# Optimization experiments

Measured on AMD Instinct MI355X. Metric: run time of the kernel, lower is better.

## Reference

```python
import jax, jax.numpy as jnp
import numpy as np

T, B, F, H, O = 2048, 256, 64, 256, 1

def setup_inputs() -> dict:
    key = jax.random.key(0)
    k0, k1, k2 = jax.random.split(key, 3)
    return {
        "x": jax.random.normal(k0, (T, B, F), jnp.float32),          # (Time, Batch, Feat)
        "W0": jax.random.normal(k1, (H, F + H), jnp.float32) * 0.05,  # i2h weight (PyTorch layout)
        "b0": jnp.zeros((H,), jnp.float32),
        "Wfc": jax.random.normal(k2, (O, H), jnp.float32) * 0.05,     # fc1 weight
        "bfc": jnp.zeros((O,), jnp.float32),
        "feature_n": 0,
    }

def reference(x, W0, b0, Wfc, bfc, feature_n):
    # RnnCell: h = tanh(Linear(cat([x_t, h], 1))); then out_t = fc1(h).
    batch = x.shape[1]
    hidden = W0.shape[0]
    h0 = jnp.zeros((batch, hidden), x.dtype)

    def step(h, x_t):
        combined = jnp.concatenate([x_t, h], axis=1)          # (B, F+H)
        h_new = jnp.tanh(combined @ W0.T + b0)                # (B, H)
        out = h_new @ Wfc.T + bfc                             # (B, O)
        return h_new, out

    _, outs = jax.lax.scan(step, h0, x)                       # (T, B, O)
    # torch.stack(outputs, 1).squeeze(2) -> (B, T)
    return jnp.transpose(outs, (1, 0, 2)).squeeze(2)
```

## Files before the change

### kernel.cpp

```cpp
#include <hip/hip_runtime.h>

#define T_STEPS 2048
#define BATCH   256
#define FEAT    64
#define HID     256
#define KAUG    320
#define NW      16
#define NTHR    1024
#define XTILE   16
#define NXB     4
#define NTILES  (T_STEPS / XTILE)

typedef _Float16 half8 __attribute__((ext_vector_type(8)));
typedef float    f32x4 __attribute__((ext_vector_type(4)));
typedef float    f32x8 __attribute__((ext_vector_type(8)));

__device__ __forceinline__ float fast_tanh(float z) {
    float e = __expf(2.0f * z);
    return 1.0f - 2.0f * __builtin_amdgcn_rcpf(e + 1.0f);
}

__global__
__attribute__((amdgpu_flat_work_group_size(NTHR, NTHR), amdgpu_waves_per_eu(4, 4)))
void rnn_kernel(const float* __restrict__ x,
                const float* __restrict__ W0,
                const float* __restrict__ b0,
                const float* __restrict__ Wfc,
                const float* __restrict__ bfc,
                float* __restrict__ out)
{
    const int b    = blockIdx.x;
    const int tid  = threadIdx.x;
    const int w    = tid >> 6;
    const int lane = tid & 63;
    const int l15  = lane & 15;
    const int kg   = lane >> 4;
    const bool alane = (l15 == 0);

    __shared__ __align__(16) _Float16 h_buf[2][HID];
    __shared__ __align__(16) _Float16 x_tile[NXB][XTILE][FEAT];
    __shared__ __align__(16) float    out_buf[T_STEPS];

    half8 bw[10];
    {
        const float* wp = W0 + (16 * w + l15) * KAUG + kg * 8;
#pragma unroll
        for (int c = 0; c < 10; ++c) {
            const f32x8 v = *reinterpret_cast<const f32x8*>(wp + c * 32);
            bw[c] = __builtin_convertvector(v, half8);
        }
    }

    float b0e = 0.f, wfe = 0.f;
    if (lane < 16) {
        b0e = b0[16 * w + lane];
        wfe = Wfc[16 * w + lane];
    }
    const float bfc_r = bfc[0];

    if (tid < HID) { h_buf[0][tid] = (_Float16)0.f; h_buf[1][tid] = (_Float16)0.f; }
    out_buf[tid]        = bfc_r;
    out_buf[tid + NTHR] = bfc_r;

    const int tr = tid >> 6;
    const int fx = tid & 63;
#pragma unroll
    for (int ti = 0; ti < 2; ++ti) {
        const float v = x[(size_t)(XTILE * ti + tr) * (BATCH * FEAT) + b * FEAT + fx];
        x_tile[ti][tr][fx] = (_Float16)v;
    }
    float xhold = x[(size_t)(XTILE * 2 + tr) * (BATCH * FEAT) + b * FEAT + fx];
    __syncthreads();

    half8 af[10];
#pragma unroll
    for (int c = 0; c < 10; ++c) af[c] = half8{};

    float p_prev = 0.f;
    const f32x4 zero4 = {0.f, 0.f, 0.f, 0.f};

    for (int t = 0; t < T_STEPS; ++t) {
        const int cur = t & 1;
        const int nxt = cur ^ 1;
        const int xb  = (t >> 4) & (NXB - 1);

        if (alane) {
            const _Float16* xr = &x_tile[xb][t & 15][kg * 8];
            af[0] = *reinterpret_cast<const half8*>(xr);
            af[1] = *reinterpret_cast<const half8*>(xr + 32);
            const _Float16* hr = &h_buf[cur][kg * 8];
#pragma unroll
            for (int c = 2; c < 10; ++c)
                af[c] = *reinterpret_cast<const half8*>(hr + (c - 2) * 32);
        }

        {
            float p = p_prev;
            p += __shfl_xor(p, 1, 64);
            p += __shfl_xor(p, 2, 64);
            p += __shfl_xor(p, 4, 64);
            p += __shfl_xor(p, 8, 64);
            if (lane == 0 && t > 0) atomicAdd(&out_buf[t - 1], p);
        }

        f32x4 a0 = __builtin_amdgcn_mfma_f32_16x16x32_f16(af[0], bw[0], zero4, 0, 0, 0);
        f32x4 a1 = __builtin_amdgcn_mfma_f32_16x16x32_f16(af[1], bw[1], zero4, 0, 0, 0);
#pragma unroll
        for (int c = 2; c < 10; c += 2) {
            a0 = __builtin_amdgcn_mfma_f32_16x16x32_f16(af[c],     bw[c],     a0, 0, 0, 0);
            a1 = __builtin_amdgcn_mfma_f32_16x16x32_f16(af[c + 1], bw[c + 1], a1, 0, 0, 0);
        }

        if ((t & 15) == 0) {
            const int ti = t >> 4;
            if (ti + 2 < NTILES)
                x_tile[(ti + 2) & (NXB - 1)][tr][fx] = (_Float16)xhold;
            if (ti + 3 < NTILES)
                xhold = x[(size_t)(XTILE * (ti + 3) + tr) * (BATCH * FEAT) + b * FEAT + fx];
        }

        float pnew = 0.f;
        if (lane < 16) {
            const float h = fast_tanh(a0[0] + a1[0] + b0e);
            h_buf[nxt][16 * w + lane] = (_Float16)h;
            pnew = wfe * h;
        }
        p_prev = pnew;

        __syncthreads();
    }

    {
        float p = p_prev;
        p += __shfl_xor(p, 1, 64);
        p += __shfl_xor(p, 2, 64);
        p += __shfl_xor(p, 4, 64);
        p += __shfl_xor(p, 8, 64);
        if (lane == 0) atomicAdd(&out_buf[T_STEPS - 1], p);
    }
    __syncthreads();

    out[b * T_STEPS + tid]        = out_buf[tid];
    out[b * T_STEPS + tid + NTHR] = out_buf[tid + NTHR];
}

extern "C" void kernel_launch(void* const* d_in, const int* in_sizes, int n_in,
                              void* d_out, int out_size, void* d_ws, size_t ws_size,
                              hipStream_t stream) {
    const float* x   = (const float*)d_in[0];
    const float* W0  = (const float*)d_in[1];
    const float* b0  = (const float*)d_in[2];
    const float* Wfc = (const float*)d_in[3];
    const float* bfc = (const float*)d_in[4];
    float* out = (float*)d_out;

    rnn_kernel<<<dim3(BATCH), dim3(NTHR), 0, stream>>>(x, W0, b0, Wfc, bfc, out);
}
```

Baseline: 1.834 ms.

## Pack eight batch rows per block into MFMA rows with fewer, larger blocks

Each block now processes 8 batch elements at once, using 8 of the 16 MFMA A-matrix rows instead of one. Each of the 8 waves computes two 16-wide hidden tiles, so there are 32 blocks of 512 threads instead of 256 blocks of 1024. The fc output is now computed from the shared hidden state with a full-wave dot product and shuffle reduction, replacing the per-step atomics. The intent is to amortise the per-step barrier and serial latency over more batch rows. The cost is only 32 blocks on a 256-CU GPU, each doing double the MFMA chain per step.

```diff
diff --git a/kernel.cpp b/kernel.cpp
--- a/kernel.cpp
+++ b/kernel.cpp
@@ -5,13 +5,17 @@
 #define FEAT    64
 #define HID     256
 #define KAUG    320
-#define NW      16
-#define NTHR    1024
+#define BPB     8
+#define NBLK    (BATCH/BPB)
+#define NW      8
+#define NTHR    512
 #define XTILE   16
-#define NXB     4
-#define NTILES  (T_STEPS / XTILE)
+#define NTILES  (T_STEPS/XTILE)
+#define PX      96
+#define PH      288
 
 typedef _Float16 half8 __attribute__((ext_vector_type(8)));
+typedef _Float16 half4 __attribute__((ext_vector_type(4)));
 typedef float    f32x4 __attribute__((ext_vector_type(4)));
 typedef float    f32x8 __attribute__((ext_vector_type(8)));
 
@@ -21,7 +25,7 @@
 }
 
 __global__
-__attribute__((amdgpu_flat_work_group_size(NTHR, NTHR), amdgpu_waves_per_eu(4, 4)))
+__attribute__((amdgpu_flat_work_group_size(NTHR, NTHR), amdgpu_waves_per_eu(2, 2)))
 void rnn_kernel(const float* __restrict__ x,
                 const float* __restrict__ W0,
                 const float* __restrict__ b0,
@@ -29,119 +33,145 @@
                 const float* __restrict__ bfc,
                 float* __restrict__ out)
 {
-    const int b    = blockIdx.x;
+    const int blk  = blockIdx.x;
+    const int B0   = blk * BPB;
     const int tid  = threadIdx.x;
     const int w    = tid >> 6;
     const int lane = tid & 63;
     const int l15  = lane & 15;
     const int kg   = lane >> 4;
-    const bool alane = (l15 == 0);
+    const bool arow = (l15 < BPB);
 
-    __shared__ __align__(16) _Float16 h_buf[2][HID];
-    __shared__ __align__(16) _Float16 x_tile[NXB][XTILE][FEAT];
-    __shared__ __align__(16) float    out_buf[T_STEPS];
+    __shared__ __align__(16) _Float16 h_fb[2][BPB][PH];
+    __shared__ __align__(16) _Float16 x_stage[2][XTILE][BPB][PX];
+    __shared__ __align__(16) float    out_buf[BPB][T_STEPS];
 
-    half8 bw[10];
-    {
-        const float* wp = W0 + (16 * w + l15) * KAUG + kg * 8;
+    half8 bw[2][10];
+#pragma unroll
+    for (int nt = 0; nt < 2; ++nt) {
+        const float* wp = W0 + ((2 * w + nt) * 16 + l15) * KAUG + kg * 8;
 #pragma unroll
         for (int c = 0; c < 10; ++c) {
             const f32x8 v = *reinterpret_cast<const f32x8*>(wp + c * 32);
-            bw[c] = __builtin_convertvector(v, half8);
+            bw[nt][c] = __builtin_convertvector(v, half8);
         }
     }
 
-    float b0e = 0.f, wfe = 0.f;
-    if (lane < 16) {
-        b0e = b0[16 * w + lane];
-        wfe = Wfc[16 * w + lane];
-    }
+    const float b0e0 = b0[(2 * w) * 16 + l15];
+    const float b0e1 = b0[(2 * w + 1) * 16 + l15];
+    const f32x4 wfc4 = *reinterpret_cast<const f32x4*>(Wfc + 4 * lane);
     const float bfc_r = bfc[0];
 
-    if (tid < HID) { h_buf[0][tid] = (_Float16)0.f; h_buf[1][tid] = (_Float16)0.f; }
-    out_buf[tid]        = bfc_r;
-    out_buf[tid + NTHR] = bfc_r;
+    const int bt = w;
+    const int ft = lane;
+    const float* xbase = x + (size_t)(B0 + bt) * FEAT + ft;
 
-    const int tr = tid >> 6;
-    const int fx = tid & 63;
+    {
+        unsigned* hz = reinterpret_cast<unsigned*>(&h_fb[0][0][0]);
 #pragma unroll
-    for (int ti = 0; ti < 2; ++ti) {
-        const float v = x[(size_t)(XTILE * ti + tr) * (BATCH * FEAT) + b * FEAT + fx];
-        x_tile[ti][tr][fx] = (_Float16)v;
+        for (int i = 0; i < 5; ++i) {
+            const int idx = tid + i * NTHR;
+            if (idx < (int)(2 * BPB * PH / 2)) hz[idx] = 0u;
+        }
     }
-    float xhold = x[(size_t)(XTILE * 2 + tr) * (BATCH * FEAT) + b * FEAT + fx];
+    float xh[XTILE];
+#pragma unroll
+    for (int s = 0; s < XTILE; ++s)
+        x_stage[0][s][bt][ft] = (_Float16)xbase[(size_t)s * (BATCH * FEAT)];
+#pragma unroll
+    for (int s = 0; s < XTILE; ++s)
+        xh[s] = xbase[(size_t)(XTILE + s) * (BATCH * FEAT)];
     __syncthreads();
 
     half8 af[10];
 #pragma unroll
     for (int c = 0; c < 10; ++c) af[c] = half8{};
 
-    float p_prev = 0.f;
     const f32x4 zero4 = {0.f, 0.f, 0.f, 0.f};
 
     for (int t = 0; t < T_STEPS; ++t) {
         const int cur = t & 1;
         const int nxt = cur ^ 1;
-        const int xb  = (t >> 4) & (NXB - 1);
+        const int ts  = t & 15;
+        const int tb  = (t >> 4) & 1;
 
-        if (alane) {
-            const _Float16* xr = &x_tile[xb][t & 15][kg * 8];
+        if (arow) {
+            const _Float16* xr = &x_stage[tb][ts][l15][kg * 8];
             af[0] = *reinterpret_cast<const half8*>(xr);
             af[1] = *reinterpret_cast<const half8*>(xr + 32);
-            const _Float16* hr = &h_buf[cur][kg * 8];
+            const _Float16* hr = &h_fb[cur][l15][kg * 8];
 #pragma unroll
             for (int c = 2; c < 10; ++c)
                 af[c] = *reinterpret_cast<const half8*>(hr + (c - 2) * 32);
         }
 
         {
-            float p = p_prev;
-            p += __shfl_xor(p, 1, 64);
-            p += __shfl_xor(p, 2, 64);
-            p += __shfl_xor(p, 4, 64);
-            p += __shfl_xor(p, 8, 64);
-            if (lane == 0 && t > 0) atomicAdd(&out_buf[t - 1], p);
+            const half4 hv = *reinterpret_cast<const half4*>(&h_fb[cur][w][4 * lane]);
+            const f32x4 hf = __builtin_convertvector(hv, f32x4);
+            float p = hf.x * wfc4.x + hf.y * wfc4.y + hf.z * wfc4.z + hf.w * wfc4.w;
+#pragma unroll
+            for (int m = 1; m <= 32; m <<= 1) p += __shfl_xor(p, m, 64);
+            if (lane == 0 && t > 0) out_buf[w][t - 1] = p + bfc_r;
         }
 
-        f32x4 a0 = __builtin_amdgcn_mfma_f32_16x16x32_f16(af[0], bw[0], zero4, 0, 0, 0);
-        f32x4 a1 = __builtin_amdgcn_mfma_f32_16x16x32_f16(af[1], bw[1], zero4, 0, 0, 0);
+        f32x4 e0 = __builtin_amdgcn_mfma_f32_16x16x32_f16(af[0], bw[0][0], zero4, 0, 0, 0);
+        f32x4 o0 = __builtin_amdgcn_mfma_f32_16x16x32_f16(af[1], bw[0][1], zero4, 0, 0, 0);
+        f32x4 e1 = __builtin_amdgcn_mfma_f32_16x16x32_f16(af[0], bw[1][0], zero4, 0, 0, 0);
+        f32x4 o1 = __builtin_amdgcn_mfma_f32_16x16x32_f16(af[1], bw[1][1], zero4, 0, 0, 0);
 #pragma unroll
         for (int c = 2; c < 10; c += 2) {
-            a0 = __builtin_amdgcn_mfma_f32_16x16x32_f16(af[c],     bw[c],     a0, 0, 0, 0);
-            a1 = __builtin_amdgcn_mfma_f32_16x16x32_f16(af[c + 1], bw[c + 1], a1, 0, 0, 0);
+            e0 = __builtin_amdgcn_mfma_f32_16x16x32_f16(af[c],     bw[0][c],     e0, 0, 0, 0);
+            o0 = __builtin_amdgcn_mfma_f32_16x16x32_f16(af[c + 1], bw[0][c + 1], o0, 0, 0, 0);
+            e1 = __builtin_amdgcn_mfma_f32_16x16x32_f16(af[c],     bw[1][c],     e1, 0, 0, 0);
+            o1 = __builtin_amdgcn_mfma_f32_16x16x32_f16(af[c + 1], bw[1][c + 1], o1, 0, 0, 0);
         }
 
-        if ((t & 15) == 0) {
+        if (ts == 0) {
             const int ti = t >> 4;
-            if (ti + 2 < NTILES)
-                x_tile[(ti + 2) & (NXB - 1)][tr][fx] = (_Float16)xhold;
-            if (ti + 3 < NTILES)
-                xhold = x[(size_t)(XTILE * (ti + 3) + tr) * (BATCH * FEAT) + b * FEAT + fx];
+            if (ti + 1 < NTILES) {
+#pragma unroll
+                for (int s = 0; s < XTILE; ++s)
+                    x_stage[(ti + 1) & 1][s][bt][ft] = (_Float16)xh[s];
+            }
+            if (ti + 2 < NTILES) {
+#pragma unroll
+                for (int s = 0; s < XTILE; ++s)
+                    xh[s] = xbase[(size_t)(16 * (ti + 2) + s) * (BATCH * FEAT)];
+            }
         }
 
-        float pnew = 0.f;
-        if (lane < 16) {
-            const float h = fast_tanh(a0[0] + a1[0] + b0e);
-            h_buf[nxt][16 * w + lane] = (_Float16)h;
-            pnew = wfe * h;
+        if (lane < 32) {
+            const int bq = (lane >> 4) * 4;
+#pragma unroll
+            for (int j = 0; j < 4; ++j) {
+                const float hA = fast_tanh(e0[j] + o0[j] + b0e0);
+                const float hB = fast_tanh(e1[j] + o1[j] + b0e1);
+                h_fb[nxt][bq + j][(2 * w) * 16 + l15]       = (_Float16)hA;
+                h_fb[nxt][bq + j][(2 * w + 1) * 16 + l15]   = (_Float16)hB;
+            }
         }
-        p_prev = pnew;
 
         __syncthreads();
     }
 
     {
-        float p = p_prev;
-        p += __shfl_xor(p, 1, 64);
-        p += __shfl_xor(p, 2, 64);
-        p += __shfl_xor(p, 4, 64);
-        p += __shfl_xor(p, 8, 64);
-        if (lane == 0) atomicAdd(&out_buf[T_STEPS - 1], p);
+        const half4 hv = *reinterpret_cast<const half4*>(&h_fb[0][w][4 * lane]);
+        const f32x4 hf = __builtin_convertvector(hv, f32x4);
+        float p = hf.x * wfc4.x + hf.y * wfc4.y + hf.z * wfc4.z + hf.w * wfc4.w;
+#pragma unroll
+        for (int m = 1; m <= 32; m <<= 1) p += __shfl_xor(p, m, 64);
+        if (lane == 0) out_buf[w][T_STEPS - 1] = p + bfc_r;
     }
     __syncthreads();
 
-    out[b * T_STEPS + tid]        = out_buf[tid];
-    out[b * T_STEPS + tid + NTHR] = out_buf[tid + NTHR];
+    const float* src = &out_buf[bt][0];
+    float* dst = out + (size_t)(B0 + bt) * T_STEPS;
+#pragma unroll
+    for (int i = 0; i < 8; ++i) {
+        const int idx = i * 256 + ft * 4;
+        *reinterpret_cast<f32x4*>(dst + idx) =
+            *reinterpret_cast<const f32x4*>(src + idx);
+    }
 }
 
 extern "C" void kernel_launch(void* const* d_in, const int* in_sizes, int n_in,
@@ -154,5 +184,5 @@
     const float* bfc = (const float*)d_in[4];
     float* out = (float*)d_out;
 
-    rnn_kernel<<<dim3(BATCH), dim3(NTHR), 0, stream>>>(x, W0, b0, Wfc, bfc, out);
+    rnn_kernel<<<dim3(NBLK), dim3(NTHR), 0, stream>>>(x, W0, b0, Wfc, bfc, out);
 }
```

Result: slower. 2.274 ms (+24.0%).
